# Kernel optimization log

Measured on AMD Instinct MI355X. Metric: run time of the kernel, lower is better.

## Reference

```python
import jax, jax.numpy as jnp
import numpy as np

N, C, P, NC, F = 1024, 256, 512, 9, 768
Q = P * (NC + 1)  # scalar output multiplicity (structurally zero: no 0e x 1o -> 0e path)


def setup_inputs():
    key = jax.random.key(0)
    ks = jax.random.split(key, 8)
    s = lambda k, shape, fan: jax.random.normal(k, shape, jnp.float32) / np.sqrt(fan)
    return {
        "encoding": jax.random.normal(ks[0], (N, 3 * C), jnp.float32),
        "W0": s(ks[1], (C, F), C), "b0": jnp.zeros((F,), jnp.float32),
        "g0": jnp.ones((F,), jnp.float32), "be0": jnp.zeros((F,), jnp.float32),
        "W1": s(ks[2], (F, F), F), "b1": jnp.zeros((F,), jnp.float32),
        "g1": jnp.ones((F,), jnp.float32), "be1": jnp.zeros((F,), jnp.float32),
        "Wout": s(ks[3], (F, C), F), "bout": jnp.zeros((C,), jnp.float32),
        "Wtp": jax.random.normal(ks[4], (C, C, P), jnp.float32),
        "num_graphs": N,
    }


def _ln(x, g, b):
    mu = jnp.mean(x, axis=-1, keepdims=True)
    var = jnp.var(x, axis=-1, keepdims=True)
    return (x - mu) * jax.lax.rsqrt(var + 1e-5) * g + b


def reference(encoding, W0, b0, g0, be0, W1, b1, g1, be1, Wout, bout, Wtp, num_graphs):
    v = encoding.reshape(num_graphs, C, 3)           # C x 1o vector features
    r = jnp.linalg.norm(v, axis=-1)                  # [N, C] rotation-invariant norms
    # radial MLP (2 hidden layers, LayerNorm + GELU), dropout=0 (eval)
    h = jax.nn.gelu(_ln(r @ W0 + b0, g0, be0))
    h = jax.nn.gelu(_ln(h @ W1 + b1, g1, be1))
    r_dec = h @ Wout + bout                          # [N, C] scalars (C x 0e)
    # FullyConnectedTensorProduct(Cx0e, Cx1o -> Px1o): uvw weights, CG(0,1,1)=I,
    # path normalization 1/sqrt(mul1*mul2) = 1/C
    t = jnp.einsum('bi,ijp->bjp', r_dec, Wtp)        # [N, C, P]
    out_vec = jnp.einsum('bjp,bjm->bpm', t, v) / C   # [N, P, 3]
    out = jnp.concatenate(
        [out_vec.reshape(num_graphs, 3 * P),
         jnp.zeros((num_graphs, Q), out_vec.dtype)], axis=-1)  # P x 1o + Q x 0e layout
    return out
```

## Files before the change

kernel.cpp:

```cpp
#include <hip/hip_runtime.h>
#include <hip/hip_bf16.h>


#define N_G   1024
#define C_DIM 256
#define P_DIM 512
#define F_DIM 768
#define OUT_STRIDE 6656
#define VEC_LEN 1536

typedef short  short8  __attribute__((ext_vector_type(8)));
typedef float  f32x16  __attribute__((ext_vector_type(16)));

#define GLOAD_LDS16(GP, LP)                                                    \
  __builtin_amdgcn_global_load_lds(                                            \
      (const __attribute__((address_space(1))) void*)(GP),                     \
      (__attribute__((address_space(3))) void*)(LP), 16, 0, 0)

static __device__ __forceinline__ unsigned short f32_bf16(float f){
  unsigned u = __builtin_bit_cast(unsigned, f);
  u = (u + 0x7fffu + ((u >> 16) & 1u)) >> 16;
  return (unsigned short)u;
}
static __device__ __forceinline__ float bf16_f32(unsigned short u){
  return __builtin_bit_cast(float, (unsigned)u << 16);
}
static __device__ __forceinline__ float gelu_tanh(float x){
  float u = 0.7978845608028654f * (x + 0.044715f * x * x * x);
  return 0.5f * x * (1.0f + tanhf(u));
}

__global__ __launch_bounds__(256) void k_prepack(const float* __restrict__ wtp,
                                                 unsigned short* __restrict__ frag){
  int tid  = blockIdx.x * 256 + threadIdx.x;
  int unit = tid >> 6, lane = tid & 63;
  int j  = unit >> 8;
  int pt = (unit >> 4) & 15;
  int ik = unit & 15;
  int p  = pt * 32 + (lane & 31);
  int i0 = ik * 16 + (lane >> 5) * 8;
  const float* src = wtp + (size_t)i0 * (C_DIM * P_DIM) + j * P_DIM + p;
  short8 v;
  #pragma unroll
  for (int e = 0; e < 8; ++e)
    v[e] = (short)f32_bf16(src[(size_t)e * (C_DIM * P_DIM)]);
  *reinterpret_cast<short8*>(frag + (size_t)unit * 512 + lane * 8) = v;
}

__global__ __launch_bounds__(256) void k_norm(const float* __restrict__ enc,
                                              float* __restrict__ r){
  int b = blockIdx.x, t = threadIdx.x;
  const float* e = enc + (size_t)b * F_DIM + t * 3;
  r[(size_t)b * C_DIM + t] = sqrtf(e[0]*e[0] + e[1]*e[1] + e[2]*e[2]);
}

__global__ __launch_bounds__(256) void k_vt(const float* __restrict__ enc,
                                            float* __restrict__ vT){
  int tid = blockIdx.x * 256 + threadIdx.x;
  int b  = tid & 1023;
  int jm = tid >> 10;
  int j  = jm / 3, m = jm - j * 3;
  vT[(size_t)j * 3072 + m * 1024 + b] = enc[(size_t)b * F_DIM + j * 3 + m];
}

template<bool OBF>
__global__ __launch_bounds__(256) void k_gemm(const float* __restrict__ A,
    const float* __restrict__ B, const float* __restrict__ bias,
    float* __restrict__ C, unsigned short* __restrict__ Cb,
    int M, int N, int K){
  __shared__ __align__(16) float Ast[64][36];
  __shared__ __align__(16) float Bs[64][64];
  int nbc = N >> 6;
  int mb = blockIdx.x / nbc, nb = blockIdx.x % nbc;
  int m0 = mb * 32, n0 = nb * 64;
  int t  = threadIdx.x;
  int tr = t >> 4, tc = t & 15;

  float acc[2][4];
  #pragma unroll
  for (int i = 0; i < 2; ++i)
    #pragma unroll
    for (int q = 0; q < 4; ++q) acc[i][q] = 0.f;

  for (int kc = 0; kc < K; kc += 64){
    {
      int m = t >> 3, k0 = (t & 7) * 8;
      const float* ap = A + (size_t)(m0 + m) * K + kc + k0;
      float4 a0 = *reinterpret_cast<const float4*>(ap);
      float4 a1 = *reinterpret_cast<const float4*>(ap + 4);
      Ast[k0+0][m] = a0.x; Ast[k0+1][m] = a0.y; Ast[k0+2][m] = a0.z; Ast[k0+3][m] = a0.w;
      Ast[k0+4][m] = a1.x; Ast[k0+5][m] = a1.y; Ast[k0+6][m] = a1.z; Ast[k0+7][m] = a1.w;
    }
    {
      int kk = t >> 2, nc = (t & 3) * 16;
      const float* bp = B + (size_t)(kc + kk) * N + n0 + nc;
      float4* d = reinterpret_cast<float4*>(&Bs[kk][nc]);
      d[0] = reinterpret_cast<const float4*>(bp)[0];
      d[1] = reinterpret_cast<const float4*>(bp)[1];
      d[2] = reinterpret_cast<const float4*>(bp)[2];
      d[3] = reinterpret_cast<const float4*>(bp)[3];
    }
    __syncthreads();
    #pragma unroll 16
    for (int kk = 0; kk < 64; ++kk){
      float2 av = *reinterpret_cast<const float2*>(&Ast[kk][tr * 2]);
      float4 bv = *reinterpret_cast<const float4*>(&Bs[kk][tc * 4]);
      acc[0][0] += av.x*bv.x; acc[0][1] += av.x*bv.y; acc[0][2] += av.x*bv.z; acc[0][3] += av.x*bv.w;
      acc[1][0] += av.y*bv.x; acc[1][1] += av.y*bv.y; acc[1][2] += av.y*bv.z; acc[1][3] += av.y*bv.w;
    }
    __syncthreads();
  }

  #pragma unroll
  for (int i = 0; i < 2; ++i){
    int row = m0 + tr * 2 + i;
    #pragma unroll
    for (int q = 0; q < 4; ++q){
      int col = n0 + tc * 4 + q;
      float val = acc[i][q] + bias[col];
      if (OBF) Cb[(size_t)row * N + col] = f32_bf16(val);
      else     C [(size_t)row * N + col] = val;
    }
  }
}

__global__ __launch_bounds__(256) void k_ln(const float* __restrict__ X,
    const float* __restrict__ g, const float* __restrict__ be,
    float* __restrict__ Y){
  int w = threadIdx.x >> 6, lane = threadIdx.x & 63;
  int row = blockIdx.x * 4 + w;
  const float* x = X + (size_t)row * F_DIM;
  float v[12];
  float s = 0.f, s2 = 0.f;
  #pragma unroll
  for (int i = 0; i < 12; ++i){
    v[i] = x[lane + i * 64];
    s += v[i]; s2 += v[i] * v[i];
  }
  #pragma unroll
  for (int off = 32; off; off >>= 1){ s += __shfl_down(s, off); s2 += __shfl_down(s2, off); }
  s = __shfl(s, 0); s2 = __shfl(s2, 0);
  float mu = s * (1.0f / F_DIM);
  float rs = rsqrtf(s2 * (1.0f / F_DIM) - mu * mu + 1e-5f);
  float* y = Y + (size_t)row * F_DIM;
  #pragma unroll
  for (int i = 0; i < 12; ++i){
    int c = lane + i * 64;
    y[c] = gelu_tanh((v[i] - mu) * rs * g[c] + be[c]);
  }
}

__global__ __launch_bounds__(512, 2) void k_tp(const unsigned short* __restrict__ frag,
    const unsigned short* __restrict__ rdec, const float* __restrict__ vT,
    unsigned short* __restrict__ part){
  __shared__ __align__(16) unsigned short As[2][16384];
  int bx   = blockIdx.x;
  int pt   = bx & 15;
  int bblk = (bx >> 4) & 3;
  int js   = bx >> 6;
  int w    = threadIdx.x >> 6;
  int lane = threadIdx.x & 63;
  int bg   = w >> 1, kh = w & 1;
  int g    = lane >> 5;
  int b0   = bblk * 256 + bg * 64 + (lane & 31);

  short8 bf[2][8];
  #pragma unroll
  for (int bt = 0; bt < 2; ++bt)
    #pragma unroll
    for (int k = 0; k < 8; ++k)
      bf[bt][k] = *reinterpret_cast<const short8*>(
          rdec + (size_t)(b0 + bt * 32) * C_DIM + (kh * 8 + k) * 16 + g * 8);

  float oacc[2][48];
  #pragma unroll
  for (int bt = 0; bt < 2; ++bt)
    #pragma unroll
    for (int q = 0; q < 48; ++q) oacc[bt][q] = 0.f;

  int j0 = js * 64;
  #define STAGE2(BUF, J) do {                                                      \
    _Pragma("unroll")                                                              \
    for (int uu = 0; uu < 4; ++uu){                                                \
      int u = w * 4 + uu;                                                          \
      const unsigned short* gp = frag +                                            \
          ((size_t)((((J) + (u >> 4)) * 16 + pt) * 16 + (u & 15))) * 512 + lane*8; \
      GLOAD_LDS16(gp, &As[BUF][u * 512]);                                          \
    } } while (0)

  STAGE2(0, j0);
  __syncthreads();
  int cur = 0;
  for (int jj = j0; jj < j0 + 64; jj += 2){
    if (jj + 2 < j0 + 64) STAGE2(cur ^ 1, jj + 2);
    #pragma unroll
    for (int jl = 0; jl < 2; ++jl){
      const unsigned short* ab = &As[cur][(jl * 16 + kh * 8) * 512 + lane * 8];
      short8 af[8];
      #pragma unroll
      for (int k = 0; k < 8; ++k)
        af[k] = *reinterpret_cast<const short8*>(ab + k * 512);
      f32x16 acc0 = {}, acc1 = {};
      #pragma unroll
      for (int k = 0; k < 8; ++k){
        acc0 = __builtin_amdgcn_mfma_f32_32x32x16_bf16(af[k], bf[0][k], acc0, 0, 0, 0);
        acc1 = __builtin_amdgcn_mfma_f32_32x32x16_bf16(af[k], bf[1][k], acc1, 0, 0, 0);
      }
      const float* vp = vT + (size_t)(jj + jl) * 3072;
      float v00 = vp[b0], v01 = vp[1024 + b0], v02 = vp[2048 + b0];
      float v10 = vp[b0 + 32], v11 = vp[1024 + b0 + 32], v12 = vp[2048 + b0 + 32];
      #pragma unroll
      for (int r = 0; r < 16; ++r){
        oacc[0][r*3+0] += acc0[r]*v00; oacc[0][r*3+1] += acc0[r]*v01; oacc[0][r*3+2] += acc0[r]*v02;
        oacc[1][r*3+0] += acc1[r]*v10; oacc[1][r*3+1] += acc1[r]*v11; oacc[1][r*3+2] += acc1[r]*v12;
      }
    }
    __syncthreads();
    cur ^= 1;
  }

  float* red = (float*)As;
  int rb = bg >> 1;
  #pragma unroll
  for (int round = 0; round < 2; ++round){
    __syncthreads();
    if (kh == 1 && rb == round){
      int chunk = (bg & 1) * 2;
      #pragma unroll
      for (int bt = 0; bt < 2; ++bt){
        float* dst = red + ((size_t)((chunk + bt) * 64 + lane)) * 48;
        #pragma unroll
        for (int q = 0; q < 48; ++q) dst[q] = oacc[bt][q];
      }
    }
    __syncthreads();
    if (kh == 0 && rb == round){
      int chunk = (bg & 1) * 2;
      #pragma unroll
      for (int bt = 0; bt < 2; ++bt){
        const float* src = red + ((size_t)((chunk + bt) * 64 + lane)) * 48;
        #pragma unroll
        for (int q = 0; q < 48; ++q) oacc[bt][q] += src[q];
      }
    }
  }
  if (kh == 0){
    #pragma unroll
    for (int bt = 0; bt < 2; ++bt){
      unsigned short* pb = part + ((size_t)js * N_G + (b0 + bt * 32)) * VEC_LEN;
      #pragma unroll
      for (int r = 0; r < 16; ++r){
        int p = pt * 32 + (r & 3) + 8 * (r >> 2) + 4 * g;
        pb[p*3+0] = f32_bf16(oacc[bt][r*3+0]);
        pb[p*3+1] = f32_bf16(oacc[bt][r*3+1]);
        pb[p*3+2] = f32_bf16(oacc[bt][r*3+2]);
      }
    }
  }
}

__global__ __launch_bounds__(256) void k_reduce(const unsigned short* __restrict__ part,
                                                float* __restrict__ out){
  int idx = blockIdx.x * 256 + threadIdx.x;
  if (idx >= N_G * OUT_STRIDE) return;
  int b = idx / OUT_STRIDE;
  int q = idx - b * OUT_STRIDE;
  float val = 0.f;
  if (q < VEC_LEN){
    size_t base = (size_t)b * VEC_LEN + q;
    const size_t st = (size_t)N_G * VEC_LEN;
    val = (bf16_f32(part[base]) + bf16_f32(part[base + st]) +
           bf16_f32(part[base + 2*st]) + bf16_f32(part[base + 3*st])) * (1.0f / C_DIM);
  }
  out[idx] = val;
}

extern "C" void kernel_launch(void* const* d_in, const int* in_sizes, int n_in,
                              void* d_out, int out_size, void* d_ws, size_t ws_size,
                              hipStream_t stream){
  const float* enc  = (const float*)d_in[0];
  const float* W0   = (const float*)d_in[1];
  const float* b0   = (const float*)d_in[2];
  const float* g0   = (const float*)d_in[3];
  const float* be0  = (const float*)d_in[4];
  const float* W1   = (const float*)d_in[5];
  const float* b1   = (const float*)d_in[6];
  const float* g1   = (const float*)d_in[7];
  const float* be1  = (const float*)d_in[8];
  const float* Wout = (const float*)d_in[9];
  const float* bout = (const float*)d_in[10];
  const float* Wtp  = (const float*)d_in[11];
  float* out = (float*)d_out;

  char* ws = (char*)d_ws;
  unsigned short* frag = (unsigned short*)(ws);
  unsigned short* rdec = (unsigned short*)(ws + 67108864);
  float*          vT   = (float*)(ws + 67633152);
  unsigned short* part = (unsigned short*)(ws + 70778880);
  float* rbuf = (float*)(ws + 70778880);
  float* bufA = (float*)(ws + 70778880 + 1048576);
  float* bufB = (float*)(ws + 70778880 + 1048576 + 3145728);

  hipLaunchKernelGGL(k_prepack, dim3(16384), dim3(256), 0, stream, Wtp, frag);
  hipLaunchKernelGGL(k_norm,    dim3(N_G),   dim3(256), 0, stream, enc, rbuf);
  hipLaunchKernelGGL(k_vt,      dim3(3072),  dim3(256), 0, stream, enc, vT);
  hipLaunchKernelGGL((k_gemm<false>), dim3(32 * 12), dim3(256), 0, stream,
                     rbuf, W0, b0, bufA, rdec, N_G, F_DIM, C_DIM);
  hipLaunchKernelGGL(k_ln,      dim3(256),   dim3(256), 0, stream, bufA, g0, be0, bufB);
  hipLaunchKernelGGL((k_gemm<false>), dim3(32 * 12), dim3(256), 0, stream,
                     bufB, W1, b1, bufA, rdec, N_G, F_DIM, F_DIM);
  hipLaunchKernelGGL(k_ln,      dim3(256),   dim3(256), 0, stream, bufA, g1, be1, bufB);
  hipLaunchKernelGGL((k_gemm<true>),  dim3(32 * 4),  dim3(256), 0, stream,
                     bufB, Wout, bout, bufA, rdec, N_G, C_DIM, F_DIM);
  hipLaunchKernelGGL(k_tp,      dim3(256),   dim3(512), 0, stream, frag, rdec, vT, part);
  hipLaunchKernelGGL(k_reduce,  dim3((N_G * OUT_STRIDE + 255) / 256), dim3(256), 0, stream,
                     part, out);
}
```

Before: 479.5 us.

## Restructure tensor-product kernel with 4-stage LDS pipeline and full-K per wave

The k_tp kernel drops the split-K across wave pairs and the LDS reduction that followed it. Each wave now owns 32 batch rows with the full 256-wide K held in registers. Fragment staging moves from a double buffer to a 4-deep ring buffer. It uses explicit vmcnt waits, raw barriers, sched barriers and setprio around the MFMA chain, and v values are prefetched in batches of 8 j's. Separately, the fp32 GEMM pads its LDS tiles differently (33/68) and uses scalar A loads, aiming to reduce bank conflicts. The hand-tuned vmcnt counts are fragile: if the count of outstanding loads is wrong, a race can occur.

Result: slower. 567.8 us (+18.4%).

```diff
diff --git a/kernel.cpp b/kernel.cpp
--- a/kernel.cpp
+++ b/kernel.cpp
@@ -68,8 +68,8 @@
     const float* __restrict__ B, const float* __restrict__ bias,
     float* __restrict__ C, unsigned short* __restrict__ Cb,
     int M, int N, int K){
-  __shared__ __align__(16) float Ast[64][36];
-  __shared__ __align__(16) float Bs[64][64];
+  __shared__ __align__(16) float Ast[64][33];
+  __shared__ __align__(16) float Bs[64][68];
   int nbc = N >> 6;
   int mb = blockIdx.x / nbc, nb = blockIdx.x % nbc;
   int m0 = mb * 32, n0 = nb * 64;
@@ -103,10 +103,10 @@
     __syncthreads();
     #pragma unroll 16
     for (int kk = 0; kk < 64; ++kk){
-      float2 av = *reinterpret_cast<const float2*>(&Ast[kk][tr * 2]);
+      float a0 = Ast[kk][tr * 2], a1 = Ast[kk][tr * 2 + 1];
       float4 bv = *reinterpret_cast<const float4*>(&Bs[kk][tc * 4]);
-      acc[0][0] += av.x*bv.x; acc[0][1] += av.x*bv.y; acc[0][2] += av.x*bv.z; acc[0][3] += av.x*bv.w;
-      acc[1][0] += av.y*bv.x; acc[1][1] += av.y*bv.y; acc[1][2] += av.y*bv.z; acc[1][3] += av.y*bv.w;
+      acc[0][0] += a0*bv.x; acc[0][1] += a0*bv.y; acc[0][2] += a0*bv.z; acc[0][3] += a0*bv.w;
+      acc[1][0] += a1*bv.x; acc[1][1] += a1*bv.y; acc[1][2] += a1*bv.z; acc[1][3] += a1*bv.w;
     }
     __syncthreads();
   }
@@ -153,109 +153,104 @@
 __global__ __launch_bounds__(512, 2) void k_tp(const unsigned short* __restrict__ frag,
     const unsigned short* __restrict__ rdec, const float* __restrict__ vT,
     unsigned short* __restrict__ part){
-  __shared__ __align__(16) unsigned short As[2][16384];
+  __shared__ __align__(16) unsigned short As[4][8192];
   int bx   = blockIdx.x;
   int pt   = bx & 15;
   int bblk = (bx >> 4) & 3;
   int js   = bx >> 6;
   int w    = threadIdx.x >> 6;
   int lane = threadIdx.x & 63;
-  int bg   = w >> 1, kh = w & 1;
   int g    = lane >> 5;
-  int b0   = bblk * 256 + bg * 64 + (lane & 31);
-
-  short8 bf[2][8];
-  #pragma unroll
-  for (int bt = 0; bt < 2; ++bt)
-    #pragma unroll
-    for (int k = 0; k < 8; ++k)
-      bf[bt][k] = *reinterpret_cast<const short8*>(
-          rdec + (size_t)(b0 + bt * 32) * C_DIM + (kh * 8 + k) * 16 + g * 8);
-
-  float oacc[2][48];
-  #pragma unroll
-  for (int bt = 0; bt < 2; ++bt)
-    #pragma unroll
-    for (int q = 0; q < 48; ++q) oacc[bt][q] = 0.f;
-
+  int b    = bblk * 256 + w * 32 + (lane & 31);
+
+  short8 bf[16];
+  #pragma unroll
+  for (int ik = 0; ik < 16; ++ik)
+    bf[ik] = *reinterpret_cast<const short8*>(rdec + (size_t)b * C_DIM + ik * 16 + g * 8);
+
+  float oacc[48];
+  #pragma unroll
+  for (int q = 0; q < 48; ++q) oacc[q] = 0.f;
+
+  float vreg[8][3];
   int j0 = js * 64;
-  #define STAGE2(BUF, J) do {                                                      \
-    _Pragma("unroll")                                                              \
-    for (int uu = 0; uu < 4; ++uu){                                                \
-      int u = w * 4 + uu;                                                          \
-      const unsigned short* gp = frag +                                            \
-          ((size_t)((((J) + (u >> 4)) * 16 + pt) * 16 + (u & 15))) * 512 + lane*8; \
-      GLOAD_LDS16(gp, &As[BUF][u * 512]);                                          \
+
+  #define STAGE(BUF, J) do {                                                        \
+    _Pragma("unroll")                                                               \
+    for (int uu = 0; uu < 2; ++uu){                                                 \
+      int u = w * 2 + uu;                                                           \
+      const unsigned short* gp = frag + ((size_t)(((J) * 16 + pt) * 16 + u)) * 512  \
+                                 + lane * 8;                                        \
+      GLOAD_LDS16(gp, &As[BUF][u * 512]);                                           \
     } } while (0)
 
-  STAGE2(0, j0);
-  __syncthreads();
-  int cur = 0;
-  for (int jj = j0; jj < j0 + 64; jj += 2){
-    if (jj + 2 < j0 + 64) STAGE2(cur ^ 1, jj + 2);
-    #pragma unroll
-    for (int jl = 0; jl < 2; ++jl){
-      const unsigned short* ab = &As[cur][(jl * 16 + kh * 8) * 512 + lane * 8];
-      short8 af[8];
-      #pragma unroll
-      for (int k = 0; k < 8; ++k)
-        af[k] = *reinterpret_cast<const short8*>(ab + k * 512);
-      f32x16 acc0 = {}, acc1 = {};
-      #pragma unroll
-      for (int k = 0; k < 8; ++k){
-        acc0 = __builtin_amdgcn_mfma_f32_32x32x16_bf16(af[k], bf[0][k], acc0, 0, 0, 0);
-        acc1 = __builtin_amdgcn_mfma_f32_32x32x16_bf16(af[k], bf[1][k], acc1, 0, 0, 0);
-      }
-      const float* vp = vT + (size_t)(jj + jl) * 3072;
-      float v00 = vp[b0], v01 = vp[1024 + b0], v02 = vp[2048 + b0];
-      float v10 = vp[b0 + 32], v11 = vp[1024 + b0 + 32], v12 = vp[2048 + b0 + 32];
-      #pragma unroll
-      for (int r = 0; r < 16; ++r){
-        oacc[0][r*3+0] += acc0[r]*v00; oacc[0][r*3+1] += acc0[r]*v01; oacc[0][r*3+2] += acc0[r]*v02;
-        oacc[1][r*3+0] += acc1[r]*v10; oacc[1][r*3+1] += acc1[r]*v11; oacc[1][r*3+2] += acc1[r]*v12;
-      }
-    }
-    __syncthreads();
-    cur ^= 1;
-  }
-
-  float* red = (float*)As;
-  int rb = bg >> 1;
-  #pragma unroll
-  for (int round = 0; round < 2; ++round){
-    __syncthreads();
-    if (kh == 1 && rb == round){
-      int chunk = (bg & 1) * 2;
-      #pragma unroll
-      for (int bt = 0; bt < 2; ++bt){
-        float* dst = red + ((size_t)((chunk + bt) * 64 + lane)) * 48;
-        #pragma unroll
-        for (int q = 0; q < 48; ++q) dst[q] = oacc[bt][q];
-      }
-    }
-    __syncthreads();
-    if (kh == 0 && rb == round){
-      int chunk = (bg & 1) * 2;
-      #pragma unroll
-      for (int bt = 0; bt < 2; ++bt){
-        const float* src = red + ((size_t)((chunk + bt) * 64 + lane)) * 48;
-        #pragma unroll
-        for (int q = 0; q < 48; ++q) oacc[bt][q] += src[q];
-      }
-    }
-  }
-  if (kh == 0){
-    #pragma unroll
-    for (int bt = 0; bt < 2; ++bt){
-      unsigned short* pb = part + ((size_t)js * N_G + (b0 + bt * 32)) * VEC_LEN;
-      #pragma unroll
-      for (int r = 0; r < 16; ++r){
-        int p = pt * 32 + (r & 3) + 8 * (r >> 2) + 4 * g;
-        pb[p*3+0] = f32_bf16(oacc[bt][r*3+0]);
-        pb[p*3+1] = f32_bf16(oacc[bt][r*3+1]);
-        pb[p*3+2] = f32_bf16(oacc[bt][r*3+2]);
-      }
-    }
+  #define VLOAD(JB) do {                                                            \
+    const float* vp_ = vT + (size_t)(JB) * 3072 + b;                                \
+    _Pragma("unroll")                                                               \
+    for (int q_ = 0; q_ < 8; ++q_){                                                 \
+      vreg[q_][0] = vp_[(size_t)q_ * 3072];                                         \
+      vreg[q_][1] = vp_[(size_t)q_ * 3072 + 1024];                                  \
+      vreg[q_][2] = vp_[(size_t)q_ * 3072 + 2048];                                  \
+    } } while (0)
+
+  #define WAITN(N) asm volatile("s_waitcnt vmcnt(" #N ")" ::: "memory")
+
+  #define TPITER(T, TQ, WN, DOSTAGE, DOVL, VJ) do {                                 \
+    WAITN(WN);                                                                      \
+    __builtin_amdgcn_s_barrier();                                                   \
+    __builtin_amdgcn_sched_barrier(0);                                              \
+    if (DOVL) VLOAD(VJ);                                                            \
+    if (DOSTAGE) STAGE(((T) + 3) & 3, j0 + (T) + 3);                                \
+    const unsigned short* ap_ = &As[(T) & 3][lane * 8];                             \
+    f32x16 acc_ = {};                                                               \
+    __builtin_amdgcn_s_setprio(1);                                                  \
+    _Pragma("unroll")                                                               \
+    for (int ik_ = 0; ik_ < 16; ++ik_){                                             \
+      short8 a_ = *reinterpret_cast<const short8*>(ap_ + (size_t)ik_ * 512);        \
+      acc_ = __builtin_amdgcn_mfma_f32_32x32x16_bf16(a_, bf[ik_], acc_, 0, 0, 0);   \
+    }                                                                               \
+    __builtin_amdgcn_s_setprio(0);                                                  \
+    _Pragma("unroll")                                                               \
+    for (int r_ = 0; r_ < 16; ++r_){                                                \
+      oacc[r_*3+0] += acc_[r_] * vreg[TQ][0];                                       \
+      oacc[r_*3+1] += acc_[r_] * vreg[TQ][1];                                       \
+      oacc[r_*3+2] += acc_[r_] * vreg[TQ][2];                                       \
+    } } while (0)
+
+  VLOAD(j0);
+  STAGE(0, j0); STAGE(1, j0 + 1); STAGE(2, j0 + 2);
+
+  TPITER(0,0,4,1,0,0); TPITER(1,1,4,1,0,0); TPITER(2,2,4,1,0,0); TPITER(3,3,4,1,0,0);
+  TPITER(4,4,4,1,0,0); TPITER(5,5,4,1,0,0); TPITER(6,6,4,1,0,0); TPITER(7,7,4,1,0,0);
+
+  for (int Gq = 1; Gq < 7; ++Gq){
+    int tb = Gq * 8;
+    TPITER(tb+0,0, 4,1,1, j0 + tb);
+    TPITER(tb+1,1,28,1,0,0);
+    TPITER(tb+2,2,28,1,0,0);
+    TPITER(tb+3,3, 4,1,0,0);
+    TPITER(tb+4,4, 4,1,0,0);
+    TPITER(tb+5,5, 4,1,0,0);
+    TPITER(tb+6,6, 4,1,0,0);
+    TPITER(tb+7,7, 4,1,0,0);
+  }
+
+  TPITER(56,0, 4,1,1, j0 + 56);
+  TPITER(57,1,28,1,0,0);
+  TPITER(58,2,28,1,0,0);
+  TPITER(59,3, 4,1,0,0);
+  TPITER(60,4, 4,1,0,0);
+  TPITER(61,5, 4,0,0,0);
+  TPITER(62,6, 2,0,0,0);
+  TPITER(63,7, 0,0,0,0);
+
+  unsigned short* pb = part + ((size_t)js * N_G + b) * VEC_LEN;
+  #pragma unroll
+  for (int r = 0; r < 16; ++r){
+    int p = pt * 32 + (r & 3) + 8 * (r >> 2) + 4 * g;
+    pb[p*3+0] = f32_bf16(oacc[r*3+0]);
+    pb[p*3+1] = f32_bf16(oacc[r*3+1]);
+    pb[p*3+2] = f32_bf16(oacc[r*3+2]);
   }
 }
 
```
